# Kernel optimization log

Measured on AMD Instinct MI355X. Metric: run time of the kernel, lower is better.

## Reference

```python
import jax, jax.numpy as jnp
import numpy as np

B, N, D, H, V, T = 128, 49, 2048, 512, 10000, 32


def setup_inputs() -> dict:
    key = jax.random.key(0)
    ks = jax.random.split(key, 12)
    s = 0.02
    return {
        "features": jax.random.normal(ks[0], (B, N, D), dtype=jnp.float32),
        "captions_in": jax.random.randint(ks[1], (B, T), 0, V),
        "embed_w": jax.random.normal(ks[2], (V, H), dtype=jnp.float32) * s,
        "W_attn_feat": jax.random.normal(ks[3], (H, D), dtype=jnp.float32) * s,
        "W_attn_h": jax.random.normal(ks[4], (H, H), dtype=jnp.float32) * s,
        "w_score": jax.random.normal(ks[5], (H,), dtype=jnp.float32) * s,
        "W_ih": jax.random.normal(ks[6], (4 * H, H + D), dtype=jnp.float32) * s,
        "W_hh": jax.random.normal(ks[7], (4 * H, H), dtype=jnp.float32) * s,
        "b_ih": jax.random.normal(ks[8], (4 * H,), dtype=jnp.float32) * s,
        "b_hh": jax.random.normal(ks[9], (4 * H,), dtype=jnp.float32) * s,
        "W_out": jax.random.normal(ks[10], (V, H), dtype=jnp.float32) * s,
        "b_out": jax.random.normal(ks[11], (V,), dtype=jnp.float32) * s,
        "sos_token": 1,
        "eos_token": 2,
        "max_len": 32,
    }


def reference(features, captions_in, embed_w, W_attn_feat, W_attn_h, w_score,
              W_ih, W_hh, b_ih, b_hh, W_out, b_out, sos_token, eos_token, max_len):
    # Teacher-forcing branch (captions_in provided); dropout in eval mode (identity).
    Bsz = features.shape[0]
    Hd = W_attn_h.shape[0]
    # feature projection is step-invariant: [B, N, H]
    proj_feat = jnp.einsum("bnd,hd->bnh", features, W_attn_feat)
    emb = embed_w[captions_in]            # [B, T, H]
    emb_t_first = jnp.swapaxes(emb, 0, 1)  # [T, B, H]
    bias = b_ih + b_hh

    def step(carry, emb_t):
        h, c = carry
        # Bahdanau attention
        ph = h @ W_attn_h.T                                   # [B, H]
        scores = jnp.tanh(proj_feat + ph[:, None, :]) @ w_score  # [B, N]
        alpha = jax.nn.softmax(scores, axis=1)
        ctx = jnp.einsum("bn,bnd->bd", alpha, features)       # [B, D]
        x = jnp.concatenate([emb_t, ctx], axis=-1)            # [B, H+D]
        # LSTMCell, torch gate order: i, f, g, o
        gates = x @ W_ih.T + h @ W_hh.T + bias                # [B, 4H]
        i, f, g, o = jnp.split(gates, 4, axis=-1)
        c_new = jax.nn.sigmoid(f) * c + jax.nn.sigmoid(i) * jnp.tanh(g)
        h_new = jax.nn.sigmoid(o) * jnp.tanh(c_new)
        logits_t = h_new @ W_out.T + b_out                    # [B, V]
        return (h_new, c_new), logits_t

    h0 = jnp.zeros((Bsz, Hd), dtype=features.dtype)
    c0 = jnp.zeros((Bsz, Hd), dtype=features.dtype)
    (h, c), logits = jax.lax.scan(step, (h0, c0), emb_t_first)
    logits = jnp.swapaxes(logits, 0, 1)  # [B, T, V]
    return logits, (h, c)
```

## Files before the change

kernel.cpp:

```cpp
#include <hip/hip_runtime.h>

typedef unsigned short u16;
typedef unsigned int u32;
typedef __attribute__((ext_vector_type(8))) short short8;
typedef __attribute__((ext_vector_type(8))) u16 u16x8;
typedef __attribute__((ext_vector_type(4))) u16 u16x4;
typedef __attribute__((ext_vector_type(4))) float f32x4;

#define DEVINL static __device__ __forceinline__

DEVINL float bf2f(u16 u) { return __uint_as_float(((u32)u) << 16); }
DEVINL u16 f2bf(float f) {
  u32 x = __float_as_uint(f);
  u32 r = (x + 0x7fffu + ((x >> 16) & 1u)) >> 16;
  return (u16)r;
}
DEVINL float fast_tanh(float x) {
  float cx = fminf(fmaxf(x, -15.f), 15.f);
  float e = __expf(2.f * cx);
  return (e - 1.f) / (e + 1.f);
}
DEVINL float sigm(float x) { return 1.f / (1.f + __expf(-x)); }

typedef __attribute__((address_space(1))) const void gvoid;
typedef __attribute__((address_space(3))) void svoid;
DEVINL void gld16(const void* g, void* l) {
  __builtin_amdgcn_global_load_lds((gvoid*)g, (svoid*)l, 16, 0, 0);
}

__global__ __launch_bounds__(256) void cast_all(
    const float* __restrict__ features, const int* __restrict__ captions,
    const float* __restrict__ embed_w, const float* __restrict__ Waf,
    const float* __restrict__ Wah, const float* __restrict__ W_ih,
    const float* __restrict__ W_hh, const float* __restrict__ b_ih,
    const float* __restrict__ b_hh, const float* __restrict__ W_out,
    u16* __restrict__ feat_bf, u16* __restrict__ Waf_bf,
    u16* __restrict__ WahT8, u16* __restrict__ Wcat, u16* __restrict__ Wemb,
    float* __restrict__ bias_perm, u16* __restrict__ Wout_bf,
    u16* __restrict__ emb_bf, u16* __restrict__ zeros_bf,
    float* __restrict__ c_state) {
  long long i = (long long)blockIdx.x * 256 + threadIdx.x;
  const long long total = 27789824LL;
  const long long stride = (long long)gridDim.x * 256;
  for (; i < total; i += stride) {
    long long r = i;
    if (r < 12845056LL) { feat_bf[r] = f2bf(features[r]); continue; }
    r -= 12845056LL;
    if (r < 1048576LL) { Waf_bf[r] = f2bf(Waf[r]); continue; }
    r -= 1048576LL;
    if (r < 262144LL) {
      long long kb = r >> 12, rem = r & 4095;
      long long row = rem >> 3, e = rem & 7;
      WahT8[r] = f2bf(Wah[row * 512 + (kb * 8 + e)]);
      continue;
    }
    r -= 262144LL;
    if (r < 5242880LL) {
      long long pr = r / 2560, k = r % 2560;
      long long o = (pr & 3) * 512 + (pr >> 2);
      float v = (k < 2048) ? W_ih[o * 2560 + 512 + k] : W_hh[o * 512 + (k - 2048)];
      Wcat[r] = f2bf(v);
      continue;
    }
    r -= 5242880LL;
    if (r < 1048576LL) {
      long long pr = r >> 9, k = r & 511;
      long long o = (pr & 3) * 512 + (pr >> 2);
      Wemb[r] = f2bf(W_ih[o * 2560 + k]);
      continue;
    }
    r -= 1048576LL;
    if (r < 2048LL) {
      long long o = (r & 3) * 512 + (r >> 2);
      bias_perm[r] = b_ih[o] + b_hh[o];
      continue;
    }
    r -= 2048LL;
    if (r < 5177344LL) {
      long long row = r >> 9, k = r & 511;
      Wout_bf[r] = (row < 10000) ? f2bf(W_out[row * 512 + k]) : (u16)0;
      continue;
    }
    r -= 5177344LL;
    if (r < 2097152LL) {
      long long m = r >> 9, k = r & 511;
      long long tt = m >> 7, b = m & 127;
      int tok = captions[b * 32 + tt];
      tok = tok < 0 ? 0 : (tok > 9999 ? 9999 : tok);
      emb_bf[r] = f2bf(embed_w[(long long)tok * 512 + k]);
      continue;
    }
    r -= 2097152LL;
    if (r < 512LL) { zeros_bf[r] = 0; continue; }
    r -= 512LL;
    c_state[r] = 0.f;
  }
}

__global__ __launch_bounds__(256) void gemm128(
    const u16* __restrict__ A, const u16* __restrict__ B,
    float* __restrict__ C, const float* __restrict__ bias,
    int K, int ldC, int Nvalid) {
  const int n0 = blockIdx.x * 128, m0 = blockIdx.y * 128;
  const int tid = threadIdx.x, w = tid >> 6, l = tid & 63;
  const int wm = w >> 1, wn = w & 1;
  __shared__ __align__(16) u16 As[2][128 * 32];
  __shared__ __align__(16) u16 Bs[2][128 * 32];
  const f32x4 z4 = {0.f, 0.f, 0.f, 0.f};
  f32x4 acc[4][4];
#pragma unroll
  for (int a_ = 0; a_ < 4; ++a_)
#pragma unroll
    for (int b_ = 0; b_ < 4; ++b_) acc[a_][b_] = z4;

  const int NT = K >> 5;
  const size_t rs = (size_t)K * 2;

  auto stage = [&](int buf, int kt) {
    const char* Ab = (const char*)A + (size_t)m0 * rs + (size_t)kt * 64;
    const char* Bb = (const char*)B + (size_t)n0 * rs + (size_t)kt * 64;
#pragma unroll
    for (int j = 0; j < 2; ++j) {
      int c = j * 256 + tid;
      int row = c >> 2, off = (c & 3) * 16;
      char* la = (char*)&As[buf][0] + (size_t)(j * 256 + w * 64) * 16;
      char* lb = (char*)&Bs[buf][0] + (size_t)(j * 256 + w * 64) * 16;
      gld16(Ab + (size_t)row * rs + off, la);
      gld16(Bb + (size_t)row * rs + off, lb);
    }
  };

  stage(0, 0);
  int cur = 0;
  const int lg = l >> 4, lr = l & 15;
  for (int kt = 0; kt < NT; ++kt) {
    __syncthreads();
    if (kt + 1 < NT) stage(cur ^ 1, kt + 1);
    short8 a[4], bb[4];
#pragma unroll
    for (int mi = 0; mi < 4; ++mi)
      a[mi] = *(const short8*)&As[cur][(wm * 64 + mi * 16 + lr) * 32 + lg * 8];
#pragma unroll
    for (int ni = 0; ni < 4; ++ni)
      bb[ni] = *(const short8*)&Bs[cur][(wn * 64 + ni * 16 + lr) * 32 + lg * 8];
#pragma unroll
    for (int mi = 0; mi < 4; ++mi)
#pragma unroll
      for (int ni = 0; ni < 4; ++ni)
        acc[mi][ni] = __builtin_amdgcn_mfma_f32_16x16x32_bf16(a[mi], bb[ni], acc[mi][ni], 0, 0, 0);
    cur ^= 1;
  }
#pragma unroll
  for (int ni = 0; ni < 4; ++ni) {
    int col = n0 + wn * 64 + ni * 16 + lr;
    if (col >= Nvalid) continue;
    float bv = bias ? bias[col] : 0.f;
#pragma unroll
    for (int mi = 0; mi < 4; ++mi) {
      int rowb = m0 + wm * 64 + mi * 16 + lg * 4;
#pragma unroll
      for (int r = 0; r < 4; ++r)
        C[(size_t)(rowb + r) * ldC + col] = acc[mi][ni][r] + bv;
    }
  }
}

__global__ __launch_bounds__(512) void attn_step(
    int t, const float* __restrict__ gates_part,
    const float* __restrict__ emb_pre,
    float* __restrict__ c_state,
    u16* __restrict__ h_all,
    const u16* __restrict__ WahT8,
    const float* __restrict__ w_score,
    const float* __restrict__ proj_feat,
    const u16* __restrict__ feat_bf,
    u16* __restrict__ ctx_bf) {
  const int b = blockIdx.x, tid = threadIdx.x;
  __shared__ float h_s[512], ph_s[512], ws_s[512];
  __shared__ float al_s[64];
  ws_s[tid] = w_score[tid];

  float hval = 0.f;
  if (t > 0) {
    const int j = tid;
    const float* gp = gates_part + (size_t)b * 2048 + 4 * j;
    const size_t ss = (size_t)128 * 2048;
    float4 g0 = *(const float4*)gp;
    float4 g1 = *(const float4*)(gp + ss);
    float4 g2 = *(const float4*)(gp + 2 * ss);
    float4 g3 = *(const float4*)(gp + 3 * ss);
    float4 ep = *(const float4*)(emb_pre + ((size_t)(t - 1) * 128 + b) * 2048 + 4 * j);
    float iv = g0.x + g1.x + g2.x + g3.x + ep.x;
    float fv = g0.y + g1.y + g2.y + g3.y + ep.y;
    float gv = g0.z + g1.z + g2.z + g3.z + ep.z;
    float ov = g0.w + g1.w + g2.w + g3.w + ep.w;
    float c_old = c_state[b * 512 + j];
    float cn = sigm(fv) * c_old + sigm(iv) * fast_tanh(gv);
    hval = sigm(ov) * fast_tanh(cn);
    c_state[b * 512 + j] = cn;
    h_all[((size_t)b * 32 + (t - 1)) * 512 + j] = f2bf(hval);
  }
  h_s[tid] = hval;
  __syncthreads();

  float ph = 0.f;
  if (t > 0) {
#pragma unroll 4
    for (int kb = 0; kb < 64; ++kb) {
      u16x8 wv = *(const u16x8*)(WahT8 + (size_t)kb * 4096 + tid * 8);
#pragma unroll
      for (int e = 0; e < 8; ++e) ph = fmaf(bf2f(wv[e]), h_s[kb * 8 + e], ph);
    }
  }
  ph_s[tid] = ph;
  __syncthreads();

  const int wv_ = tid >> 6, ln = tid & 63;
  for (int n = wv_; n < 49; n += 8) {
    const float* pf = proj_feat + ((size_t)b * 49 + n) * 512 + ln * 8;
    float4 p0 = *(const float4*)pf;
    float4 p1 = *(const float4*)(pf + 4);
    const int k0 = ln * 8;
    float s;
    s  = fast_tanh(p0.x + ph_s[k0 + 0]) * ws_s[k0 + 0];
    s += fast_tanh(p0.y + ph_s[k0 + 1]) * ws_s[k0 + 1];
    s += fast_tanh(p0.z + ph_s[k0 + 2]) * ws_s[k0 + 2];
    s += fast_tanh(p0.w + ph_s[k0 + 3]) * ws_s[k0 + 3];
    s += fast_tanh(p1.x + ph_s[k0 + 4]) * ws_s[k0 + 4];
    s += fast_tanh(p1.y + ph_s[k0 + 5]) * ws_s[k0 + 5];
    s += fast_tanh(p1.z + ph_s[k0 + 6]) * ws_s[k0 + 6];
    s += fast_tanh(p1.w + ph_s[k0 + 7]) * ws_s[k0 + 7];
#pragma unroll
    for (int off = 32; off > 0; off >>= 1) s += __shfl_down(s, off);
    if (ln == 0) al_s[n] = s;
  }
  __syncthreads();
  if (tid < 64) {
    float v = (tid < 49) ? al_s[tid] : -1e30f;
    float m = v;
#pragma unroll
    for (int off = 32; off > 0; off >>= 1) m = fmaxf(m, __shfl_xor(m, off));
    float e = (tid < 49) ? __expf(v - m) : 0.f;
    float sm = e;
#pragma unroll
    for (int off = 32; off > 0; off >>= 1) sm += __shfl_xor(sm, off);
    if (tid < 49) al_s[tid] = e / sm;
  }
  __syncthreads();

  float c0 = 0, c1 = 0, c2 = 0, c3 = 0;
  const u16* fb = feat_bf + (size_t)b * 49 * 2048 + tid * 4;
  for (int n = 0; n < 49; ++n) {
    float a = al_s[n];
    u16x4 v = *(const u16x4*)(fb + (size_t)n * 2048);
    c0 = fmaf(bf2f(v[0]), a, c0);
    c1 = fmaf(bf2f(v[1]), a, c1);
    c2 = fmaf(bf2f(v[2]), a, c2);
    c3 = fmaf(bf2f(v[3]), a, c3);
  }
  u16x4 o;
  o[0] = f2bf(c0); o[1] = f2bf(c1); o[2] = f2bf(c2); o[3] = f2bf(c3);
  *(u16x4*)(ctx_bf + (size_t)b * 2048 + tid * 4) = o;
}

__global__ __launch_bounds__(256) void gates_step(
    int t, const u16* __restrict__ ctx_bf,
    const u16* __restrict__ h_all,
    const u16* __restrict__ zeros_bf,
    const u16* __restrict__ Wcat,
    float* __restrict__ gates_part) {
  const int ns = blockIdx.x, bt = blockIdx.y, ks = blockIdx.z;
  const int b0 = bt * 32, row0 = ns * 128;
  const int tid = threadIdx.x, w = tid >> 6, l = tid & 63;
  __shared__ __align__(16) u16 Xs[2][32 * 64];
  __shared__ __align__(16) u16 Ws[2][128 * 64];
  const f32x4 z4 = {0.f, 0.f, 0.f, 0.f};
  f32x4 acc[2][2];
  acc[0][0] = z4; acc[0][1] = z4; acc[1][0] = z4; acc[1][1] = z4;

  auto stage = [&](int buf, int kt) {
    {
      int c = tid;
      int lrow = c >> 3;
      int kb = ks * 1280 + kt * 128 + (((c & 7) * 16) ^ ((lrow & 7) << 4));
      const char* g;
      if (kb < 4096)
        g = (const char*)ctx_bf + (size_t)(b0 + lrow) * 4096 + kb;
      else if (t > 0)
        g = (const char*)h_all + ((size_t)(b0 + lrow) * 32 + (t - 1)) * 1024 + (kb - 4096);
      else
        g = (const char*)zeros_bf + (kb - 4096);
      gld16(g, (char*)&Xs[buf][0] + (size_t)(w * 64) * 16);
    }
#pragma unroll
    for (int j = 0; j < 4; ++j) {
      int c = j * 256 + tid;
      int lrow = c >> 3;
      int kb = ks * 1280 + kt * 128 + (((c & 7) * 16) ^ ((lrow & 7) << 4));
      const char* g = (const char*)Wcat + (size_t)(row0 + lrow) * 5120 + kb;
      gld16(g, (char*)&Ws[buf][0] + (size_t)(j * 256 + w * 64) * 16);
    }
  };

  stage(0, 0);
  int cur = 0;
  const int lg = l >> 4, lr = l & 15;
  for (int kt = 0; kt < 10; ++kt) {
    __syncthreads();
    if (kt + 1 < 10) stage(cur ^ 1, kt + 1);
#pragma unroll
    for (int k2 = 0; k2 < 2; ++k2) {
      short8 a[2], bb[2];
#pragma unroll
      for (int mi = 0; mi < 2; ++mi) {
        int lrow = mi * 16 + lr;
        int off = (k2 * 64 + lg * 16) ^ ((lrow & 7) << 4);
        a[mi] = *(const short8*)((const char*)&Xs[cur][0] + lrow * 128 + off);
      }
#pragma unroll
      for (int ni = 0; ni < 2; ++ni) {
        int lrow = w * 32 + ni * 16 + lr;
        int off = (k2 * 64 + lg * 16) ^ ((lrow & 7) << 4);
        bb[ni] = *(const short8*)((const char*)&Ws[cur][0] + lrow * 128 + off);
      }
#pragma unroll
      for (int mi = 0; mi < 2; ++mi)
#pragma unroll
        for (int ni = 0; ni < 2; ++ni)
          acc[mi][ni] = __builtin_amdgcn_mfma_f32_16x16x32_bf16(a[mi], bb[ni], acc[mi][ni], 0, 0, 0);
    }
    cur ^= 1;
  }
  float* gp = gates_part + (size_t)ks * 128 * 2048;
#pragma unroll
  for (int mi = 0; mi < 2; ++mi)
#pragma unroll
    for (int ni = 0; ni < 2; ++ni) {
      int col = row0 + w * 32 + ni * 16 + lr;
#pragma unroll
      for (int r = 0; r < 4; ++r) {
        int m = b0 + mi * 16 + lg * 4 + r;
        gp[(size_t)m * 2048 + col] = acc[mi][ni][r];
      }
    }
}

__global__ __launch_bounds__(512) void final_update(
    const float* __restrict__ gates_part, const float* __restrict__ emb_pre_t,
    float* __restrict__ c_state, u16* __restrict__ h_all,
    float* __restrict__ out_h, float* __restrict__ out_c) {
  const int b = blockIdx.x, j = threadIdx.x;
  const float* gp = gates_part + (size_t)b * 2048 + 4 * j;
  const size_t ss = (size_t)128 * 2048;
  float4 g0 = *(const float4*)gp;
  float4 g1 = *(const float4*)(gp + ss);
  float4 g2 = *(const float4*)(gp + 2 * ss);
  float4 g3 = *(const float4*)(gp + 3 * ss);
  float4 ep = *(const float4*)(emb_pre_t + (size_t)b * 2048 + 4 * j);
  float iv = g0.x + g1.x + g2.x + g3.x + ep.x;
  float fv = g0.y + g1.y + g2.y + g3.y + ep.y;
  float gv = g0.z + g1.z + g2.z + g3.z + ep.z;
  float ov = g0.w + g1.w + g2.w + g3.w + ep.w;
  float c_old = c_state[b * 512 + j];
  float cn = sigm(fv) * c_old + sigm(iv) * fast_tanh(gv);
  float hval = sigm(ov) * fast_tanh(cn);
  out_h[b * 512 + j] = hval;
  out_c[b * 512 + j] = cn;
  h_all[((size_t)b * 32 + 31) * 512 + j] = f2bf(hval);
}

extern "C" void kernel_launch(void* const* d_in, const int* in_sizes, int n_in,
                              void* d_out, int out_size, void* d_ws, size_t ws_size,
                              hipStream_t stream) {
  (void)in_sizes; (void)n_in; (void)out_size; (void)ws_size;
  const float* features = (const float*)d_in[0];
  const int*   captions = (const int*)d_in[1];
  const float* embed_w  = (const float*)d_in[2];
  const float* Waf      = (const float*)d_in[3];
  const float* Wah      = (const float*)d_in[4];
  const float* w_score  = (const float*)d_in[5];
  const float* W_ih     = (const float*)d_in[6];
  const float* W_hh     = (const float*)d_in[7];
  const float* b_ih     = (const float*)d_in[8];
  const float* b_hh     = (const float*)d_in[9];
  const float* W_out    = (const float*)d_in[10];
  const float* b_out    = (const float*)d_in[11];

  float* out = (float*)d_out;
  u16*   feat_bf   = (u16*)out;
  float* proj_feat = out + 6422528;
  float* emb_pre   = out + 9633792;
  u16*   Wcat      = (u16*)(out + 18022400);
  u16*   Waf_bf    = (u16*)(out + 20643840);
  u16*   WahT8     = (u16*)(out + 21168128);
  u16*   Wemb      = (u16*)(out + 21299200);
  float* bias_perm = out + 21823488;
  u16*   emb_bf    = (u16*)(out + 21825536);
  float* out_h     = out + 40960000;
  float* out_c     = out_h + 65536;

  char* wsp = (char*)d_ws;
  u16*   Wout_bf    = (u16*)wsp;  wsp += 10354688;
  u16*   h_all      = (u16*)wsp;  wsp += 4194304;
  u16*   ctx_bf     = (u16*)wsp;  wsp += 524288;
  float* gates_part = (float*)wsp; wsp += 4194304;
  float* c_state    = (float*)wsp; wsp += 262144;
  u16*   zeros_bf   = (u16*)wsp;  wsp += 1024;

  cast_all<<<8192, 256, 0, stream>>>(features, captions, embed_w, Waf, Wah,
      W_ih, W_hh, b_ih, b_hh, W_out, feat_bf, Waf_bf, WahT8, Wcat, Wemb,
      bias_perm, Wout_bf, emb_bf, zeros_bf, c_state);

  gemm128<<<dim3(4, 49), 256, 0, stream>>>(feat_bf, Waf_bf, proj_feat,
                                           nullptr, 2048, 512, 512);
  gemm128<<<dim3(16, 32), 256, 0, stream>>>(emb_bf, Wemb, emb_pre,
                                            bias_perm, 512, 2048, 2048);

  for (int t = 0; t < 32; ++t) {
    attn_step<<<128, 512, 0, stream>>>(t, gates_part, emb_pre, c_state, h_all,
                                       WahT8, w_score, proj_feat, feat_bf, ctx_bf);
    gates_step<<<dim3(16, 4, 4), 256, 0, stream>>>(t, ctx_bf, h_all, zeros_bf,
                                                   Wcat, gates_part);
  }
  final_update<<<128, 512, 0, stream>>>(gates_part,
      emb_pre + (size_t)31 * 128 * 2048, c_state, h_all, out_h, out_c);

  gemm128<<<dim3(79, 32), 256, 0, stream>>>(h_all, Wout_bf, out,
                                            b_out, 512, 10000, 10000);
}
```

Measured before the change: 1.269 ms.

## Fuse decode steps into one persistent cooperative kernel with grid barriers

```diff
diff --git a/kernel.cpp b/kernel.cpp
--- a/kernel.cpp
+++ b/kernel.cpp
@@ -26,6 +26,24 @@
 typedef __attribute__((address_space(3))) void svoid;
 DEVINL void gld16(const void* g, void* l) {
   __builtin_amdgcn_global_load_lds((gvoid*)g, (svoid*)l, 16, 0, 0);
+}
+
+DEVINL void gridbar(u32* bar, u32 nblk) {
+  __syncthreads();
+  if (threadIdx.x == 0) {
+    volatile u32* gen = bar + 1;
+    u32 g = *gen;
+    __threadfence();
+    if (atomicAdd(bar, 1u) == nblk - 1) {
+      atomicExch(bar, 0u);
+      __threadfence();
+      atomicAdd((u32*)(bar + 1), 1u);
+    } else {
+      while (*gen == g) __builtin_amdgcn_s_sleep(2);
+    }
+    __threadfence();
+  }
+  __syncthreads();
 }
 
 __global__ __launch_bounds__(256) void cast_all(
@@ -38,9 +56,9 @@
     u16* __restrict__ WahT8, u16* __restrict__ Wcat, u16* __restrict__ Wemb,
     float* __restrict__ bias_perm, u16* __restrict__ Wout_bf,
     u16* __restrict__ emb_bf, u16* __restrict__ zeros_bf,
-    float* __restrict__ c_state) {
+    u32* __restrict__ bar) {
   long long i = (long long)blockIdx.x * 256 + threadIdx.x;
-  const long long total = 27789824LL;
+  const long long total = 27789826LL;
   const long long stride = (long long)gridDim.x * 256;
   for (; i < total; i += stride) {
     long long r = i;
@@ -76,12 +94,12 @@
       continue;
     }
     r -= 2048LL;
-    if (r < 5177344LL) {
+    if (r < 5242880LL) {
       long long row = r >> 9, k = r & 511;
       Wout_bf[r] = (row < 10000) ? f2bf(W_out[row * 512 + k]) : (u16)0;
       continue;
     }
-    r -= 5177344LL;
+    r -= 5242880LL;
     if (r < 2097152LL) {
       long long m = r >> 9, k = r & 511;
       long long tt = m >> 7, b = m & 127;
@@ -93,7 +111,7 @@
     r -= 2097152LL;
     if (r < 512LL) { zeros_bf[r] = 0; continue; }
     r -= 512LL;
-    c_state[r] = 0.f;
+    bar[r] = 0u;
   }
 }
 
@@ -122,7 +140,7 @@
 #pragma unroll
     for (int j = 0; j < 2; ++j) {
       int c = j * 256 + tid;
-      int row = c >> 2, off = (c & 3) * 16;
+      int row = c >> 2, off = ((c & 3) * 16) ^ ((row & 3) << 4);
       char* la = (char*)&As[buf][0] + (size_t)(j * 256 + w * 64) * 16;
       char* lb = (char*)&Bs[buf][0] + (size_t)(j * 256 + w * 64) * 16;
       gld16(Ab + (size_t)row * rs + off, la);
@@ -138,11 +156,15 @@
     if (kt + 1 < NT) stage(cur ^ 1, kt + 1);
     short8 a[4], bb[4];
 #pragma unroll
-    for (int mi = 0; mi < 4; ++mi)
-      a[mi] = *(const short8*)&As[cur][(wm * 64 + mi * 16 + lr) * 32 + lg * 8];
-#pragma unroll
-    for (int ni = 0; ni < 4; ++ni)
-      bb[ni] = *(const short8*)&Bs[cur][(wn * 64 + ni * 16 + lr) * 32 + lg * 8];
+    for (int mi = 0; mi < 4; ++mi) {
+      int row = wm * 64 + mi * 16 + lr;
+      a[mi] = *(const short8*)((const char*)&As[cur][0] + (size_t)row * 64 + ((lg * 16) ^ ((row & 3) << 4)));
+    }
+#pragma unroll
+    for (int ni = 0; ni < 4; ++ni) {
+      int row = wn * 64 + ni * 16 + lr;
+      bb[ni] = *(const short8*)((const char*)&Bs[cur][0] + (size_t)row * 64 + ((lg * 16) ^ ((row & 3) << 4)));
+    }
 #pragma unroll
     for (int mi = 0; mi < 4; ++mi)
 #pragma unroll
@@ -165,208 +187,262 @@
   }
 }
 
-__global__ __launch_bounds__(512) void attn_step(
-    int t, const float* __restrict__ gates_part,
-    const float* __restrict__ emb_pre,
-    float* __restrict__ c_state,
-    u16* __restrict__ h_all,
-    const u16* __restrict__ WahT8,
-    const float* __restrict__ w_score,
-    const float* __restrict__ proj_feat,
-    const u16* __restrict__ feat_bf,
-    u16* __restrict__ ctx_bf) {
-  const int b = blockIdx.x, tid = threadIdx.x;
-  __shared__ float h_s[512], ph_s[512], ws_s[512];
-  __shared__ float al_s[64];
-  ws_s[tid] = w_score[tid];
-
-  float hval = 0.f;
-  if (t > 0) {
-    const int j = tid;
-    const float* gp = gates_part + (size_t)b * 2048 + 4 * j;
-    const size_t ss = (size_t)128 * 2048;
-    float4 g0 = *(const float4*)gp;
-    float4 g1 = *(const float4*)(gp + ss);
-    float4 g2 = *(const float4*)(gp + 2 * ss);
-    float4 g3 = *(const float4*)(gp + 3 * ss);
-    float4 ep = *(const float4*)(emb_pre + ((size_t)(t - 1) * 128 + b) * 2048 + 4 * j);
-    float iv = g0.x + g1.x + g2.x + g3.x + ep.x;
-    float fv = g0.y + g1.y + g2.y + g3.y + ep.y;
-    float gv = g0.z + g1.z + g2.z + g3.z + ep.z;
-    float ov = g0.w + g1.w + g2.w + g3.w + ep.w;
-    float c_old = c_state[b * 512 + j];
-    float cn = sigm(fv) * c_old + sigm(iv) * fast_tanh(gv);
-    hval = sigm(ov) * fast_tanh(cn);
-    c_state[b * 512 + j] = cn;
-    h_all[((size_t)b * 32 + (t - 1)) * 512 + j] = f2bf(hval);
-  }
-  h_s[tid] = hval;
-  __syncthreads();
-
-  float ph = 0.f;
-  if (t > 0) {
-#pragma unroll 4
-    for (int kb = 0; kb < 64; ++kb) {
-      u16x8 wv = *(const u16x8*)(WahT8 + (size_t)kb * 4096 + tid * 8);
-#pragma unroll
-      for (int e = 0; e < 8; ++e) ph = fmaf(bf2f(wv[e]), h_s[kb * 8 + e], ph);
-    }
-  }
-  ph_s[tid] = ph;
-  __syncthreads();
-
-  const int wv_ = tid >> 6, ln = tid & 63;
-  for (int n = wv_; n < 49; n += 8) {
-    const float* pf = proj_feat + ((size_t)b * 49 + n) * 512 + ln * 8;
-    float4 p0 = *(const float4*)pf;
-    float4 p1 = *(const float4*)(pf + 4);
-    const int k0 = ln * 8;
-    float s;
-    s  = fast_tanh(p0.x + ph_s[k0 + 0]) * ws_s[k0 + 0];
-    s += fast_tanh(p0.y + ph_s[k0 + 1]) * ws_s[k0 + 1];
-    s += fast_tanh(p0.z + ph_s[k0 + 2]) * ws_s[k0 + 2];
-    s += fast_tanh(p0.w + ph_s[k0 + 3]) * ws_s[k0 + 3];
-    s += fast_tanh(p1.x + ph_s[k0 + 4]) * ws_s[k0 + 4];
-    s += fast_tanh(p1.y + ph_s[k0 + 5]) * ws_s[k0 + 5];
-    s += fast_tanh(p1.z + ph_s[k0 + 6]) * ws_s[k0 + 6];
-    s += fast_tanh(p1.w + ph_s[k0 + 7]) * ws_s[k0 + 7];
-#pragma unroll
-    for (int off = 32; off > 0; off >>= 1) s += __shfl_down(s, off);
-    if (ln == 0) al_s[n] = s;
-  }
-  __syncthreads();
-  if (tid < 64) {
-    float v = (tid < 49) ? al_s[tid] : -1e30f;
-    float m = v;
-#pragma unroll
-    for (int off = 32; off > 0; off >>= 1) m = fmaxf(m, __shfl_xor(m, off));
-    float e = (tid < 49) ? __expf(v - m) : 0.f;
-    float sm = e;
-#pragma unroll
-    for (int off = 32; off > 0; off >>= 1) sm += __shfl_xor(sm, off);
-    if (tid < 49) al_s[tid] = e / sm;
-  }
-  __syncthreads();
-
-  float c0 = 0, c1 = 0, c2 = 0, c3 = 0;
-  const u16* fb = feat_bf + (size_t)b * 49 * 2048 + tid * 4;
-  for (int n = 0; n < 49; ++n) {
-    float a = al_s[n];
-    u16x4 v = *(const u16x4*)(fb + (size_t)n * 2048);
-    c0 = fmaf(bf2f(v[0]), a, c0);
-    c1 = fmaf(bf2f(v[1]), a, c1);
-    c2 = fmaf(bf2f(v[2]), a, c2);
-    c3 = fmaf(bf2f(v[3]), a, c3);
-  }
-  u16x4 o;
-  o[0] = f2bf(c0); o[1] = f2bf(c1); o[2] = f2bf(c2); o[3] = f2bf(c3);
-  *(u16x4*)(ctx_bf + (size_t)b * 2048 + tid * 4) = o;
-}
-
-__global__ __launch_bounds__(256) void gates_step(
-    int t, const u16* __restrict__ ctx_bf,
-    const u16* __restrict__ h_all,
-    const u16* __restrict__ zeros_bf,
-    const u16* __restrict__ Wcat,
-    float* __restrict__ gates_part) {
-  const int ns = blockIdx.x, bt = blockIdx.y, ks = blockIdx.z;
-  const int b0 = bt * 32, row0 = ns * 128;
+__global__ __launch_bounds__(256) void gemm_logits(
+    const u16* __restrict__ A, const u16* __restrict__ B,
+    float* __restrict__ C, const float* __restrict__ bias) {
+  const int id = blockIdx.x;
+  const int k8 = id & 7, j2 = id >> 3;
+  const int n0 = (k8 * 10 + (j2 % 10)) * 128;
+  const int m0 = (j2 / 10) * 128;
   const int tid = threadIdx.x, w = tid >> 6, l = tid & 63;
-  __shared__ __align__(16) u16 Xs[2][32 * 64];
-  __shared__ __align__(16) u16 Ws[2][128 * 64];
+  const int wm = w >> 1, wn = w & 1;
+  __shared__ __align__(16) u16 As[2][128 * 32];
+  __shared__ __align__(16) u16 Bs[2][128 * 32];
   const f32x4 z4 = {0.f, 0.f, 0.f, 0.f};
-  f32x4 acc[2][2];
-  acc[0][0] = z4; acc[0][1] = z4; acc[1][0] = z4; acc[1][1] = z4;
+  f32x4 acc[4][4];
+#pragma unroll
+  for (int a_ = 0; a_ < 4; ++a_)
+#pragma unroll
+    for (int b_ = 0; b_ < 4; ++b_) acc[a_][b_] = z4;
+
+  const size_t rs = 1024;
 
   auto stage = [&](int buf, int kt) {
-    {
-      int c = tid;
-      int lrow = c >> 3;
-      int kb = ks * 1280 + kt * 128 + (((c & 7) * 16) ^ ((lrow & 7) << 4));
-      const char* g;
-      if (kb < 4096)
-        g = (const char*)ctx_bf + (size_t)(b0 + lrow) * 4096 + kb;
-      else if (t > 0)
-        g = (const char*)h_all + ((size_t)(b0 + lrow) * 32 + (t - 1)) * 1024 + (kb - 4096);
-      else
-        g = (const char*)zeros_bf + (kb - 4096);
-      gld16(g, (char*)&Xs[buf][0] + (size_t)(w * 64) * 16);
-    }
-#pragma unroll
-    for (int j = 0; j < 4; ++j) {
+    const char* Ab = (const char*)A + (size_t)m0 * rs + (size_t)kt * 64;
+    const char* Bb = (const char*)B + (size_t)n0 * rs + (size_t)kt * 64;
+#pragma unroll
+    for (int j = 0; j < 2; ++j) {
       int c = j * 256 + tid;
-      int lrow = c >> 3;
-      int kb = ks * 1280 + kt * 128 + (((c & 7) * 16) ^ ((lrow & 7) << 4));
-      const char* g = (const char*)Wcat + (size_t)(row0 + lrow) * 5120 + kb;
-      gld16(g, (char*)&Ws[buf][0] + (size_t)(j * 256 + w * 64) * 16);
+      int row = c >> 2, off = ((c & 3) * 16) ^ ((row & 3) << 4);
+      char* la = (char*)&As[buf][0] + (size_t)(j * 256 + w * 64) * 16;
+      char* lb = (char*)&Bs[buf][0] + (size_t)(j * 256 + w * 64) * 16;
+      gld16(Ab + (size_t)row * rs + off, la);
+      gld16(Bb + (size_t)row * rs + off, lb);
     }
   };
 
   stage(0, 0);
   int cur = 0;
   const int lg = l >> 4, lr = l & 15;
-  for (int kt = 0; kt < 10; ++kt) {
+  for (int kt = 0; kt < 16; ++kt) {
     __syncthreads();
-    if (kt + 1 < 10) stage(cur ^ 1, kt + 1);
-#pragma unroll
-    for (int k2 = 0; k2 < 2; ++k2) {
-      short8 a[2], bb[2];
-#pragma unroll
-      for (int mi = 0; mi < 2; ++mi) {
-        int lrow = mi * 16 + lr;
-        int off = (k2 * 64 + lg * 16) ^ ((lrow & 7) << 4);
-        a[mi] = *(const short8*)((const char*)&Xs[cur][0] + lrow * 128 + off);
+    if (kt + 1 < 16) stage(cur ^ 1, kt + 1);
+    short8 a[4], bb[4];
+#pragma unroll
+    for (int mi = 0; mi < 4; ++mi) {
+      int row = wm * 64 + mi * 16 + lr;
+      a[mi] = *(const short8*)((const char*)&As[cur][0] + (size_t)row * 64 + ((lg * 16) ^ ((row & 3) << 4)));
+    }
+#pragma unroll
+    for (int ni = 0; ni < 4; ++ni) {
+      int row = wn * 64 + ni * 16 + lr;
+      bb[ni] = *(const short8*)((const char*)&Bs[cur][0] + (size_t)row * 64 + ((lg * 16) ^ ((row & 3) << 4)));
+    }
+#pragma unroll
+    for (int mi = 0; mi < 4; ++mi)
+#pragma unroll
+      for (int ni = 0; ni < 4; ++ni)
+        acc[mi][ni] = __builtin_amdgcn_mfma_f32_16x16x32_bf16(a[mi], bb[ni], acc[mi][ni], 0, 0, 0);
+    cur ^= 1;
+  }
+#pragma unroll
+  for (int ni = 0; ni < 4; ++ni) {
+    int col = n0 + wn * 64 + ni * 16 + lr;
+    if (col >= 10000) continue;
+    float bv = bias[col];
+#pragma unroll
+    for (int mi = 0; mi < 4; ++mi) {
+      int rowb = m0 + wm * 64 + mi * 16 + lg * 4;
+#pragma unroll
+      for (int r = 0; r < 4; ++r)
+        C[(size_t)(rowb + r) * 10000 + col] = acc[mi][ni][r] + bv;
+    }
+  }
+}
+
+struct LoopArgs {
+  float* gates_part;
+  const float* emb_pre;
+  u16* h_all;
+  const u16* WahT8;
+  const float* w_score;
+  const float* proj_feat;
+  const u16* feat_bf;
+  u16* ctx_bf;
+  const u16* Wcat;
+  const u16* zeros_bf;
+  float* out_h;
+  float* out_c;
+  u32* bar;
+};
+
+__global__ __launch_bounds__(512, 1) void decode_loop(LoopArgs A) {
+  const int blk = blockIdx.x, tid = threadIdx.x;
+  const int b = blk;
+  const int ns = blk >> 3, ks = blk & 7;
+  const int w = tid >> 6, l = tid & 63;
+  const int lg = l >> 4, lr = l & 15;
+  const int wm = w >> 2, wn = w & 3;
+  __shared__ float c_s[512], h_s[512], ph_s[512], ws_s[512];
+  __shared__ float al_s[64];
+  __shared__ __align__(16) u16 Xs[2][128 * 64];
+  __shared__ __align__(16) u16 Ws[2][128 * 64];
+  c_s[tid] = 0.f;
+  ws_s[tid] = A.w_score[tid];
+
+  for (int t = 0; t <= 32; ++t) {
+    float hval = 0.f;
+    if (t > 0) {
+      const int j = tid;
+      const size_t ss = (size_t)128 * 2048;
+      const float* gp = A.gates_part + (size_t)b * 2048 + 4 * j;
+      float4 s = *(const float4*)(A.emb_pre + ((size_t)(t - 1) * 128 + b) * 2048 + 4 * j);
+#pragma unroll
+      for (int p = 0; p < 8; ++p) {
+        float4 g = *(const float4*)(gp + p * ss);
+        s.x += g.x; s.y += g.y; s.z += g.z; s.w += g.w;
       }
+      float c_old = c_s[j];
+      float cn = sigm(s.y) * c_old + sigm(s.x) * fast_tanh(s.z);
+      hval = sigm(s.w) * fast_tanh(cn);
+      c_s[j] = cn;
+      A.h_all[((size_t)b * 32 + (t - 1)) * 512 + j] = f2bf(hval);
+      if (t == 32) { A.out_h[b * 512 + j] = hval; A.out_c[b * 512 + j] = cn; }
+    }
+    h_s[tid] = hval;
+    __syncthreads();
+    if (t == 32) break;
+
+    float ph = 0.f;
+    if (t > 0) {
+#pragma unroll 4
+      for (int kb = 0; kb < 64; ++kb) {
+        u16x8 wv = *(const u16x8*)(A.WahT8 + (size_t)kb * 4096 + tid * 8);
+#pragma unroll
+        for (int e = 0; e < 8; ++e) ph = fmaf(bf2f(wv[e]), h_s[kb * 8 + e], ph);
+      }
+    }
+    ph_s[tid] = ph;
+    __syncthreads();
+
+    for (int n = w; n < 49; n += 8) {
+      const float* pf = A.proj_feat + ((size_t)b * 49 + n) * 512 + l * 8;
+      float4 p0 = *(const float4*)pf;
+      float4 p1 = *(const float4*)(pf + 4);
+      const int k0 = l * 8;
+      float s;
+      s  = fast_tanh(p0.x + ph_s[k0 + 0]) * ws_s[k0 + 0];
+      s += fast_tanh(p0.y + ph_s[k0 + 1]) * ws_s[k0 + 1];
+      s += fast_tanh(p0.z + ph_s[k0 + 2]) * ws_s[k0 + 2];
+      s += fast_tanh(p0.w + ph_s[k0 + 3]) * ws_s[k0 + 3];
+      s += fast_tanh(p1.x + ph_s[k0 + 4]) * ws_s[k0 + 4];
+      s += fast_tanh(p1.y + ph_s[k0 + 5]) * ws_s[k0 + 5];
+      s += fast_tanh(p1.z + ph_s[k0 + 6]) * ws_s[k0 + 6];
+      s += fast_tanh(p1.w + ph_s[k0 + 7]) * ws_s[k0 + 7];
+#pragma unroll
+      for (int off = 32; off > 0; off >>= 1) s += __shfl_down(s, off);
+      if (l == 0) al_s[n] = s;
+    }
+    __syncthreads();
+    if (tid < 64) {
+      float v = (tid < 49) ? al_s[tid] : -1e30f;
+      float m = v;
+#pragma unroll
+      for (int off = 32; off > 0; off >>= 1) m = fmaxf(m, __shfl_xor(m, off));
+      float e = (tid < 49) ? __expf(v - m) : 0.f;
+      float sm = e;
+#pragma unroll
+      for (int off = 32; off > 0; off >>= 1) sm += __shfl_xor(sm, off);
+      if (tid < 49) al_s[tid] = e / sm;
+    }
+    __syncthreads();
+
+    {
+      float c0 = 0, c1 = 0, c2 = 0, c3 = 0;
+      const u16* fb = A.feat_bf + (size_t)b * 49 * 2048 + tid * 4;
+      for (int n = 0; n < 49; ++n) {
+        float a = al_s[n];
+        u16x4 v = *(const u16x4*)(fb + (size_t)n * 2048);
+        c0 = fmaf(bf2f(v[0]), a, c0);
+        c1 = fmaf(bf2f(v[1]), a, c1);
+        c2 = fmaf(bf2f(v[2]), a, c2);
+        c3 = fmaf(bf2f(v[3]), a, c3);
+      }
+      u16x4 o;
+      o[0] = f2bf(c0); o[1] = f2bf(c1); o[2] = f2bf(c2); o[3] = f2bf(c3);
+      *(u16x4*)(A.ctx_bf + (size_t)b * 2048 + tid * 4) = o;
+    }
+
+    gridbar(A.bar, 128);
+
+    const f32x4 z4 = {0.f, 0.f, 0.f, 0.f};
+    f32x4 acc[4][2];
+#pragma unroll
+    for (int mi = 0; mi < 4; ++mi) { acc[mi][0] = z4; acc[mi][1] = z4; }
+
+    auto stageB = [&](int buf, int kt) {
+      const int kbase = ks * 640 + kt * 128;
+#pragma unroll
+      for (int it = 0; it < 2; ++it) {
+        int c = it * 512 + tid;
+        int row = c >> 3;
+        int colb = kbase + (((c & 7) * 16) ^ ((row & 7) << 4));
+        const char* g;
+        if (colb < 4096)
+          g = (const char*)A.ctx_bf + (size_t)row * 4096 + colb;
+        else if (t > 0)
+          g = (const char*)A.h_all + ((size_t)row * 32 + (t - 1)) * 1024 + (colb - 4096);
+        else
+          g = (const char*)A.zeros_bf + (colb - 4096);
+        gld16(g, (char*)&Xs[buf][0] + (size_t)(it * 512 + w * 64) * 16);
+        const char* gw = (const char*)A.Wcat + (size_t)(ns * 128 + row) * 5120 + colb;
+        gld16(gw, (char*)&Ws[buf][0] + (size_t)(it * 512 + w * 64) * 16);
+      }
+    };
+
+    stageB(0, 0);
+    int cur = 0;
+    for (int kt = 0; kt < 5; ++kt) {
+      __syncthreads();
+      if (kt + 1 < 5) stageB(cur ^ 1, kt + 1);
+#pragma unroll
+      for (int k2 = 0; k2 < 2; ++k2) {
+        short8 av[4], bv[2];
+#pragma unroll
+        for (int mi = 0; mi < 4; ++mi) {
+          int row = wm * 64 + mi * 16 + lr;
+          av[mi] = *(const short8*)((const char*)&Xs[cur][0] + (size_t)row * 128 +
+                                    ((k2 * 64 + lg * 16) ^ ((row & 7) << 4)));
+        }
+#pragma unroll
+        for (int ni = 0; ni < 2; ++ni) {
+          int row = wn * 32 + ni * 16 + lr;
+          bv[ni] = *(const short8*)((const char*)&Ws[cur][0] + (size_t)row * 128 +
+                                    ((k2 * 64 + lg * 16) ^ ((row & 7) << 4)));
+        }
+#pragma unroll
+        for (int mi = 0; mi < 4; ++mi)
+#pragma unroll
+          for (int ni = 0; ni < 2; ++ni)
+            acc[mi][ni] = __builtin_amdgcn_mfma_f32_16x16x32_bf16(av[mi], bv[ni], acc[mi][ni], 0, 0, 0);
+      }
+      cur ^= 1;
+    }
+    float* gp = A.gates_part + (size_t)ks * 128 * 2048;
+#pragma unroll
+    for (int mi = 0; mi < 4; ++mi)
 #pragma unroll
       for (int ni = 0; ni < 2; ++ni) {
-        int lrow = w * 32 + ni * 16 + lr;
-        int off = (k2 * 64 + lg * 16) ^ ((lrow & 7) << 4);
-        bb[ni] = *(const short8*)((const char*)&Ws[cur][0] + lrow * 128 + off);
+        int col = ns * 128 + wn * 32 + ni * 16 + lr;
+#pragma unroll
+        for (int r = 0; r < 4; ++r) {
+          int m = wm * 64 + mi * 16 + lg * 4 + r;
+          gp[(size_t)m * 2048 + col] = acc[mi][ni][r];
+        }
       }
-#pragma unroll
-      for (int mi = 0; mi < 2; ++mi)
-#pragma unroll
-        for (int ni = 0; ni < 2; ++ni)
-          acc[mi][ni] = __builtin_amdgcn_mfma_f32_16x16x32_bf16(a[mi], bb[ni], acc[mi][ni], 0, 0, 0);
-    }
-    cur ^= 1;
-  }
-  float* gp = gates_part + (size_t)ks * 128 * 2048;
-#pragma unroll
-  for (int mi = 0; mi < 2; ++mi)
-#pragma unroll
-    for (int ni = 0; ni < 2; ++ni) {
-      int col = row0 + w * 32 + ni * 16 + lr;
-#pragma unroll
-      for (int r = 0; r < 4; ++r) {
-        int m = b0 + mi * 16 + lg * 4 + r;
-        gp[(size_t)m * 2048 + col] = acc[mi][ni][r];
-      }
-    }
-}
-
-__global__ __launch_bounds__(512) void final_update(
-    const float* __restrict__ gates_part, const float* __restrict__ emb_pre_t,
-    float* __restrict__ c_state, u16* __restrict__ h_all,
-    float* __restrict__ out_h, float* __restrict__ out_c) {
-  const int b = blockIdx.x, j = threadIdx.x;
-  const float* gp = gates_part + (size_t)b * 2048 + 4 * j;
-  const size_t ss = (size_t)128 * 2048;
-  float4 g0 = *(const float4*)gp;
-  float4 g1 = *(const float4*)(gp + ss);
-  float4 g2 = *(const float4*)(gp + 2 * ss);
-  float4 g3 = *(const float4*)(gp + 3 * ss);
-  float4 ep = *(const float4*)(emb_pre_t + (size_t)b * 2048 + 4 * j);
-  float iv = g0.x + g1.x + g2.x + g3.x + ep.x;
-  float fv = g0.y + g1.y + g2.y + g3.y + ep.y;
-  float gv = g0.z + g1.z + g2.z + g3.z + ep.z;
-  float ov = g0.w + g1.w + g2.w + g3.w + ep.w;
-  float c_old = c_state[b * 512 + j];
-  float cn = sigm(fv) * c_old + sigm(iv) * fast_tanh(gv);
-  float hval = sigm(ov) * fast_tanh(cn);
-  out_h[b * 512 + j] = hval;
-  out_c[b * 512 + j] = cn;
-  h_all[((size_t)b * 32 + 31) * 512 + j] = f2bf(hval);
+
+    gridbar(A.bar, 128);
+  }
 }
 
 extern "C" void kernel_launch(void* const* d_in, const int* in_sizes, int n_in,
@@ -396,35 +472,34 @@
   u16*   Wemb      = (u16*)(out + 21299200);
   float* bias_perm = out + 21823488;
   u16*   emb_bf    = (u16*)(out + 21825536);
+  float* gates_part= out + 22874112;
+  u16*   ctx_bf    = (u16*)(out + 24971264);
   float* out_h     = out + 40960000;
   float* out_c     = out_h + 65536;
 
   char* wsp = (char*)d_ws;
-  u16*   Wout_bf    = (u16*)wsp;  wsp += 10354688;
-  u16*   h_all      = (u16*)wsp;  wsp += 4194304;
-  u16*   ctx_bf     = (u16*)wsp;  wsp += 524288;
-  float* gates_part = (float*)wsp; wsp += 4194304;
-  float* c_state    = (float*)wsp; wsp += 262144;
-  u16*   zeros_bf   = (u16*)wsp;  wsp += 1024;
+  u16*   Wout_bf = (u16*)wsp;  wsp += 10485760;
+  u16*   h_all   = (u16*)wsp;  wsp += 4194304;
+  u16*   zeros_bf= (u16*)wsp;  wsp += 1024;
+  u32*   bar     = (u32*)wsp;  wsp += 8;
 
   cast_all<<<8192, 256, 0, stream>>>(features, captions, embed_w, Waf, Wah,
       W_ih, W_hh, b_ih, b_hh, W_out, feat_bf, Waf_bf, WahT8, Wcat, Wemb,
-      bias_perm, Wout_bf, emb_bf, zeros_bf, c_state);
+      bias_perm, Wout_bf, emb_bf, zeros_bf, bar);
 
   gemm128<<<dim3(4, 49), 256, 0, stream>>>(feat_bf, Waf_bf, proj_feat,
                                            nullptr, 2048, 512, 512);
   gemm128<<<dim3(16, 32), 256, 0, stream>>>(emb_bf, Wemb, emb_pre,
                                             bias_perm, 512, 2048, 2048);
 
-  for (int t = 0; t < 32; ++t) {
-    attn_step<<<128, 512, 0, stream>>>(t, gates_part, emb_pre, c_state, h_all,
-                                       WahT8, w_score, proj_feat, feat_bf, ctx_bf);
-    gates_step<<<dim3(16, 4, 4), 256, 0, stream>>>(t, ctx_bf, h_all, zeros_bf,
-                                                   Wcat, gates_part);
-  }
-  final_update<<<128, 512, 0, stream>>>(gates_part,
-      emb_pre + (size_t)31 * 128 * 2048, c_state, h_all, out_h, out_c);
-
-  gemm128<<<dim3(79, 32), 256, 0, stream>>>(h_all, Wout_bf, out,
-                                            b_out, 512, 10000, 10000);
-}
+  LoopArgs la;
+  la.gates_part = gates_part; la.emb_pre = emb_pre; la.h_all = h_all;
+  la.WahT8 = WahT8; la.w_score = w_score; la.proj_feat = proj_feat;
+  la.feat_bf = feat_bf; la.ctx_bf = ctx_bf; la.Wcat = Wcat;
+  la.zeros_bf = zeros_bf; la.out_h = out_h; la.out_c = out_c; la.bar = bar;
+  void* kargs[] = { (void*)&la };
+  hipLaunchCooperativeKernel((const void*)decode_loop, dim3(128), dim3(512),
+                             kargs, 0, stream);
+
+  gemm_logits<<<2560, 256, 0, stream>>>(h_all, Wout_bf, out, b_out);
+}
```

Result: slower. 2.830 ms (+123.0%).
